# Optimization experiments

Measured on AMD Instinct MI355X. Metric: run time of the kernel, lower is better.

The kernel has to match this reference:

```python
import jax, jax.numpy as jnp
import numpy as np

GROUPS = 32
HEADS = 8
EPS = 1e-5


def group_norm(x, w, b):
    B, C, H, W = x.shape
    xg = x.reshape(B, GROUPS, C // GROUPS, H, W)
    mu = xg.mean(axis=(2, 3, 4), keepdims=True)
    var = xg.var(axis=(2, 3, 4), keepdims=True)
    xn = ((xg - mu) * jax.lax.rsqrt(var + EPS)).reshape(B, C, H, W)
    return xn * w[None, :, None, None] + b[None, :, None, None]


def conv1x1(x, w, b):
    # w: [out_c, in_c], x: [B, C, H, W]
    return jnp.einsum('oc,bchw->bohw', w, x) + b[None, :, None, None]


def setup_inputs() -> dict:
    key = jax.random.key(0)
    ks = jax.random.split(key, 10)
    B, C, H, W = 8, 512, 32, 32
    s = 1.0 / np.sqrt(C)
    inp = {
        'x': jax.random.normal(ks[0], (B, C, H, W), dtype=jnp.float32),
        'gn_w': jnp.ones((C,), jnp.float32),
        'gn_b': jnp.zeros((C,), jnp.float32),
        'qw': jax.random.uniform(ks[1], (C, C), jnp.float32, -s, s),
        'qb': jax.random.uniform(ks[2], (C,), jnp.float32, -s, s),
        'kw': jax.random.uniform(ks[3], (C, C), jnp.float32, -s, s),
        'kb': jax.random.uniform(ks[4], (C,), jnp.float32, -s, s),
        'vw': jax.random.uniform(ks[5], (C, C), jnp.float32, -s, s),
        'vb': jax.random.uniform(ks[6], (C,), jnp.float32, -s, s),
        'ow': jax.random.uniform(ks[7], (C, C), jnp.float32, -s, s),
        'ob': jax.random.uniform(ks[8], (C,), jnp.float32, -s, s),
    }
    return inp


def reference(x, gn_w, gn_b, qw, qb, kw, kb, vw, vb, ow, ob):
    B, C, H, W = x.shape
    hd = C // HEADS          # head_dim
    N = H * W                # spatial tokens
    scale = float(hd) ** -0.5

    xn = group_norm(x, gn_w, gn_b)
    q = conv1x1(xn, qw, qb).reshape(B, HEADS, hd, N)
    k = conv1x1(xn, kw, kb).reshape(B, HEADS, hd, N)
    v = conv1x1(xn, vw, vb).reshape(B, HEADS, hd, N)

    # scores[b,h,n,m] = scale * <q[:, :, :, n], k[:, :, :, m]>
    scores = jnp.einsum('bhdn,bhdm->bhnm', q * scale, k)
    attn = jax.nn.softmax(scores, axis=-1)
    # out[b,h,d,n] = sum_m attn[b,h,n,m] * v[b,h,d,m]
    out = jnp.einsum('bhnm,bhdm->bhdn', attn, v).reshape(B, C, H, W)
    out = conv1x1(out, ow, ob)
    return out + x
```

## Files before the change

kernel.cpp:

```cpp
#include <hip/hip_runtime.h>
#include <cstdint>


typedef unsigned short u16;
typedef __attribute__((ext_vector_type(8))) __bf16 bf16x8;
typedef __attribute__((ext_vector_type(4))) __bf16 bf16x4;
typedef __attribute__((ext_vector_type(4))) float  f32x4;

typedef __attribute__((address_space(1))) const unsigned int guint;
typedef __attribute__((address_space(3))) unsigned int       luint;

__device__ __forceinline__ u16 f2bf(float f) {
  union { float f; unsigned u; } a; a.f = f;
  unsigned r = a.u + 0x7fffu + ((a.u >> 16) & 1u);
  return (u16)(r >> 16);
}

__device__ __forceinline__ void gload16(u16* lds_dst, const u16* g_src) {
  __builtin_amdgcn_global_load_lds((guint*)g_src, (luint*)lds_dst, 16, 0, 0);
}

__global__ __launch_bounds__(256) void gn_stats(const float* __restrict__ x,
                                                float* __restrict__ pstat) {
  int id = blockIdx.x;
  int bg = id >> 1, chunk = id & 1;
  int b = bg >> 5, g = bg & 31;
  int tid = threadIdx.x;
  const float* xg = x + ((size_t)(b * 512 + g * 16 + chunk * 8)) * 1024;
  float s1 = 0.f, s2 = 0.f;
#pragma unroll
  for (int it = 0; it < 8; ++it) {
    f32x4 v = *(const f32x4*)(xg + it * 1024 + tid * 4);
    s1 += (v[0] + v[1]) + (v[2] + v[3]);
    s2 += (v[0] * v[0] + v[1] * v[1]) + (v[2] * v[2] + v[3] * v[3]);
  }
#pragma unroll
  for (int d = 32; d; d >>= 1) { s1 += __shfl_down(s1, d, 64); s2 += __shfl_down(s2, d, 64); }
  __shared__ float redw[4][2];
  if ((tid & 63) == 0) { redw[tid >> 6][0] = s1; redw[tid >> 6][1] = s2; }
  __syncthreads();
  if (tid == 0) {
    float t1 = redw[0][0] + redw[1][0] + redw[2][0] + redw[3][0];
    float t2 = redw[0][1] + redw[1][1] + redw[2][1] + redw[3][1];
    pstat[(bg * 2 + chunk) * 2 + 0] = t1;
    pstat[(bg * 2 + chunk) * 2 + 1] = t2;
  }
}

__global__ __launch_bounds__(256) void gn_apply(const float* __restrict__ x,
                                                const float* __restrict__ pstat,
                                                const float* __restrict__ gw,
                                                const float* __restrict__ gb,
                                                u16* __restrict__ xnT) {
  __shared__ u16 tr[64 * 130];
  int id = blockIdx.x;
  int cs = id & 3, ntl = (id >> 2) & 15, b = id >> 6;
  int tid = threadIdx.x;
  int tc = tid >> 1, th = tid & 1;
  int c = cs * 128 + tc, g = c >> 4;
  float a1 = pstat[(b * 32 + g) * 4 + 0], a2 = pstat[(b * 32 + g) * 4 + 1];
  float b1 = pstat[(b * 32 + g) * 4 + 2], b2 = pstat[(b * 32 + g) * 4 + 3];
  float s1 = a1 + b1, s2 = a2 + b2;
  float mean = s1 * (1.f / 16384.f);
  float var  = s2 * (1.f / 16384.f) - mean * mean;
  float rinv = rsqrtf(var + 1e-5f);
  float wgt = gw[c] * rinv;
  float bia = gb[c] - mean * wgt;
  const float* src = x + ((size_t)(b * 512 + c)) * 1024 + ntl * 64 + th * 32;
#pragma unroll
  for (int i = 0; i < 8; ++i) {
    f32x4 v = *(const f32x4*)(src + i * 4);
#pragma unroll
    for (int j = 0; j < 4; ++j)
      tr[(th * 32 + i * 4 + j) * 130 + tc] = f2bf(v[j] * wgt + bia);
  }
  __syncthreads();
  int n = tid >> 2, q = tid & 3;
  u16* dst = xnT + (size_t)b * 524288 + (size_t)(ntl * 64 + n) * 512 + cs * 128 + q * 32;
#pragma unroll
  for (int wd = 0; wd < 16; ++wd)
    *(unsigned*)&dst[wd * 2] = *(const unsigned*)&tr[n * 130 + q * 32 + wd * 2];
}

__global__ __launch_bounds__(256) void cvtw_kernel(const float* __restrict__ q,
                                                   const float* __restrict__ k,
                                                   const float* __restrict__ v,
                                                   const float* __restrict__ o,
                                                   u16* __restrict__ dst) {
  int i = blockIdx.x * 256 + threadIdx.x;
  int wsel = i >> 16;
  const float* src = wsel == 0 ? q : wsel == 1 ? k : wsel == 2 ? v : o;
  f32x4 val = *(const f32x4*)(src + (size_t)(i & 65535) * 4);
  u16 r0 = f2bf(val[0]), r1 = f2bf(val[1]), r2 = f2bf(val[2]), r3 = f2bf(val[3]);
  unsigned lo = (unsigned)r0 | ((unsigned)r1 << 16);
  unsigned hi = (unsigned)r2 | ((unsigned)r3 << 16);
  unsigned long long pk = (unsigned long long)lo | ((unsigned long long)hi << 32);
  *(unsigned long long*)(dst + (size_t)i * 4) = pk;
}

__global__ __launch_bounds__(256) void gemm_qkv(
    const u16* __restrict__ xnT, const u16* __restrict__ Wc,
    const float* __restrict__ qb, const float* __restrict__ kb,
    const float* __restrict__ vb,
    u16* __restrict__ Qs, u16* __restrict__ Ks, u16* __restrict__ Vs) {
  __shared__ u16 smem[32768];
  int id = blockIdx.x;
  int xcd = id & 7, slot = id >> 3;
  int g12 = slot / 12, q12 = slot % 12;
  int p = xcd * 8 + g12;
  int b = p & 7, yt = p >> 3;
  int xt = q12 & 3, which = q12 >> 2;

  const u16* Ab = xnT + (size_t)b * 524288 + (size_t)yt * 128 * 512;
  const u16* Bb = Wc + which * 262144 + (size_t)xt * 128 * 512;
  const float* bias = which == 0 ? qb : (which == 1 ? kb : vb);
  float scale = which == 0 ? 0.18033688011112043f : 1.0f;

  int tid = threadIdx.x, w = tid >> 6, lane = tid & 63;
  int wr = w >> 1, wcn = w & 1;
  int srow = lane >> 3, sk8 = (lane & 7) ^ srow;
  f32x4 acc[4][4] = {};

#define QKV_STAGE(buf, k0)                                                     \
  {                                                                            \
    u16* lA_ = smem + (buf) * 8192;                                            \
    u16* lB_ = smem + 16384 + (buf) * 8192;                                    \
    _Pragma("unroll")                                                          \
    for (int c2 = 0; c2 < 4; ++c2) {                                           \
      int ck = w * 4 + c2;                                                     \
      gload16(&lA_[ck * 512], Ab + (size_t)(ck * 8 + srow) * 512 + (k0) + sk8 * 8); \
      gload16(&lB_[ck * 512], Bb + (size_t)(ck * 8 + srow) * 512 + (k0) + sk8 * 8); \
    }                                                                          \
  }

  QKV_STAGE(0, 0);
  __syncthreads();
  for (int t = 0; t < 8; ++t) {
    if (t < 7) QKV_STAGE((t + 1) & 1, (t + 1) * 64);
    const u16* lA = smem + (t & 1) * 8192;
    const u16* lB = smem + 16384 + (t & 1) * 8192;
#pragma unroll
    for (int ks = 0; ks < 2; ++ks) {
      int k8 = ks * 4 + (lane >> 4);
      bf16x8 af[4], bfr[4];
#pragma unroll
      for (int mf = 0; mf < 4; ++mf) {
        int row = wr * 64 + mf * 16 + (lane & 15);
        af[mf] = *(const bf16x8*)&lA[row * 64 + ((k8 ^ (row & 7)) * 8)];
      }
#pragma unroll
      for (int nf = 0; nf < 4; ++nf) {
        int row = wcn * 64 + nf * 16 + (lane & 15);
        bfr[nf] = *(const bf16x8*)&lB[row * 64 + ((k8 ^ (row & 7)) * 8)];
      }
#pragma unroll
      for (int mf = 0; mf < 4; ++mf)
#pragma unroll
        for (int nf = 0; nf < 4; ++nf)
          acc[mf][nf] = __builtin_amdgcn_mfma_f32_16x16x32_bf16(af[mf], bfr[nf], acc[mf][nf], 0, 0, 0);
    }
    __syncthreads();
  }
#undef QKV_STAGE

  if (which < 2) {
    u16* dst = (which == 0 ? Qs : Ks) + (size_t)b * 524288;
#pragma unroll
    for (int mf = 0; mf < 4; ++mf)
#pragma unroll
      for (int nf = 0; nf < 4; ++nf) {
        int cc = xt * 128 + wcn * 64 + nf * 16 + (lane & 15);
        float bv = bias[cc];
#pragma unroll
        for (int j = 0; j < 4; ++j) {
          int rr = yt * 128 + wr * 64 + mf * 16 + (lane >> 4) * 4 + j;
          dst[(size_t)rr * 512 + cc] = f2bf((acc[mf][nf][j] + bv) * scale);
        }
      }
  } else {
    u16* tr = smem;
#pragma unroll
    for (int mf = 0; mf < 4; ++mf)
#pragma unroll
      for (int nf = 0; nf < 4; ++nf) {
        int cc_t = wcn * 64 + nf * 16 + (lane & 15);
        float bv = bias[xt * 128 + cc_t];
#pragma unroll
        for (int j = 0; j < 4; ++j) {
          int rr_t = wr * 64 + mf * 16 + (lane >> 4) * 4 + j;
          tr[cc_t * 136 + rr_t] = f2bf(acc[mf][nf][j] + bv);
        }
      }
    __syncthreads();
    int r = tid >> 1, half = tid & 1;
    size_t base = (size_t)b * 524288 + (size_t)(xt * 128 + r) * 1024 + yt * 128 + half * 64;
#pragma unroll
    for (int i = 0; i < 8; ++i) {
      bf16x8 v = *(const bf16x8*)&tr[r * 136 + half * 64 + i * 8];
      *(bf16x8*)&Vs[base + i * 8] = v;
    }
  }
}

__global__ __launch_bounds__(256) void attn_kernel(const u16* __restrict__ Q,
                                                   const u16* __restrict__ Kt,
                                                   const u16* __restrict__ V,
                                                   u16* __restrict__ AO) {
  __shared__ __align__(16) u16 lK[2][4096];
  __shared__ __align__(16) u16 lV[2][4096];
  __shared__ __align__(16) u16 plds[4][2048];
  int id = blockIdx.x;
  int xcd = id & 7, slot = id >> 3;
  int bh = xcd * 8 + (slot >> 3);
  int nt = slot & 7;
  int b = bh >> 3, h = bh & 7;
  int tid = threadIdx.x, w = tid >> 6, lane = tid & 63;
  int ln = lane & 15, hi = lane >> 4;
  int nb = nt * 128 + w * 32;
  const u16* Qb = Q  + (size_t)b * 524288;
  const u16* Kb = Kt + (size_t)b * 524288 + h * 64;
  const u16* Vb = V  + (size_t)b * 524288 + (size_t)(h * 64) * 1024;
  char* pw = (char*)&plds[w][0];
  int srow = lane >> 3, sk8 = (lane & 7) ^ srow;

  int kidx[2][4];
#pragma unroll
  for (int ks = 0; ks < 2; ++ks)
#pragma unroll
    for (int xf = 0; xf < 4; ++xf) {
      int row = xf * 16 + ln;
      kidx[ks][xf] = row * 64 + (((ks * 4 + hi) ^ (row & 7)) * 8);
    }
  int woff[4], roff[2];
#pragma unroll
  for (int nf = 0; nf < 4; ++nf)
    woff[nf] = ln * 128 + ((nf * 32 + hi * 8) ^ ((ln & 7) << 4));
#pragma unroll
  for (int ks = 0; ks < 2; ++ks)
    roff[ks] = ln * 128 + ((ks * 64 + hi * 16) ^ ((ln & 7) << 4));

  bf16x8 bq[2][2];
#pragma unroll
  for (int nq = 0; nq < 2; ++nq)
#pragma unroll
    for (int ks = 0; ks < 2; ++ks)
      bq[nq][ks] = *(const bf16x8*)&Qb[(size_t)(nb + nq * 16 + ln) * 512 +
                                       h * 64 + ks * 32 + hi * 8];

  f32x4 o[2][4] = {};
  float lp[2] = {0.f, 0.f};

#define ATTN_STAGE(buf, m0)                                                    \
  {                                                                            \
    _Pragma("unroll")                                                          \
    for (int c2 = 0; c2 < 2; ++c2) {                                           \
      int ck = w * 2 + c2;                                                     \
      gload16(&lK[buf][ck * 512], Kb + (size_t)((m0) + ck * 8 + srow) * 512 + sk8 * 8); \
      gload16(&lV[buf][ck * 512], Vb + (size_t)(ck * 8 + srow) * 1024 + (m0) + sk8 * 8); \
    }                                                                          \
  }

  ATTN_STAGE(0, 0);
  __syncthreads();
  for (int mt = 0; mt < 16; ++mt) {
    int cur = mt & 1;
    if (mt < 15) ATTN_STAGE(cur ^ 1, (mt + 1) * 64);
    f32x4 s[2][4] = {};
#pragma unroll
    for (int ks = 0; ks < 2; ++ks) {
#pragma unroll
      for (int nf = 0; nf < 4; ++nf) {
        bf16x8 ak = *(const bf16x8*)&lK[cur][kidx[ks][nf]];
        s[0][nf] = __builtin_amdgcn_mfma_f32_16x16x32_bf16(ak, bq[0][ks], s[0][nf], 0, 0, 0);
        s[1][nf] = __builtin_amdgcn_mfma_f32_16x16x32_bf16(ak, bq[1][ks], s[1][nf], 0, 0, 0);
      }
    }
#pragma unroll
    for (int nq = 0; nq < 2; ++nq)
#pragma unroll
      for (int nf = 0; nf < 4; ++nf) {
        float p0 = exp2f(s[nq][nf][0]), p1 = exp2f(s[nq][nf][1]);
        float p2 = exp2f(s[nq][nf][2]), p3 = exp2f(s[nq][nf][3]);
        lp[nq] += (p0 + p1) + (p2 + p3);
        bf16x4 pb;
        pb[0] = (__bf16)p0; pb[1] = (__bf16)p1; pb[2] = (__bf16)p2; pb[3] = (__bf16)p3;
        *(bf16x4*)(pw + nq * 2048 + woff[nf]) = pb;
      }
#pragma unroll
    for (int ks = 0; ks < 2; ++ks) {
      bf16x8 ap0 = *(const bf16x8*)(pw + roff[ks]);
      bf16x8 ap1 = *(const bf16x8*)(pw + 2048 + roff[ks]);
#pragma unroll
      for (int df = 0; df < 4; ++df) {
        bf16x8 bv = *(const bf16x8*)&lV[cur][kidx[ks][df]];
        o[0][df] = __builtin_amdgcn_mfma_f32_16x16x32_bf16(ap0, bv, o[0][df], 0, 0, 0);
        o[1][df] = __builtin_amdgcn_mfma_f32_16x16x32_bf16(ap1, bv, o[1][df], 0, 0, 0);
      }
    }
    __syncthreads();
  }
#undef ATTN_STAGE

#pragma unroll
  for (int nq = 0; nq < 2; ++nq) {
    lp[nq] += __shfl_xor(lp[nq], 16, 64);
    lp[nq] += __shfl_xor(lp[nq], 32, 64);
  }
  float* lf = (float*)pw;
  if (hi == 0) { lf[ln] = lp[0]; lf[16 + ln] = lp[1]; }
  f32x4 lv0 = *(const f32x4*)&lf[hi * 4];
  f32x4 lv1 = *(const f32x4*)&lf[16 + hi * 4];
  float rl[2][4];
#pragma unroll
  for (int j = 0; j < 4; ++j) { rl[0][j] = 1.0f / lv0[j]; rl[1][j] = 1.0f / lv1[j]; }

#pragma unroll
  for (int nq = 0; nq < 2; ++nq)
#pragma unroll
    for (int df = 0; df < 4; ++df)
#pragma unroll
      for (int j = 0; j < 4; ++j) {
        int n = nb + nq * 16 + hi * 4 + j;
        int c = h * 64 + df * 16 + ln;
        AO[(size_t)b * 524288 + (size_t)n * 512 + c] = f2bf(o[nq][df][j] * rl[nq][j]);
      }
}

__global__ __launch_bounds__(256) void gemm_proj(
    const u16* __restrict__ Wo, const u16* __restrict__ AO,
    const float* __restrict__ ob, const float* __restrict__ x,
    float* __restrict__ out) {
  __shared__ u16 smem[24576];
  int id = blockIdx.x;
  int xcd = id & 7, slot = id >> 3;
  int g8 = slot >> 3, y = slot & 7;
  int p = xcd * 8 + g8;
  int b = p & 7, xt = p >> 3;

  const u16* Ab = Wo + (size_t)y * 64 * 512;
  const u16* Bb = AO + (size_t)b * 524288 + (size_t)xt * 128 * 512;

  int tid = threadIdx.x, w = tid >> 6, lane = tid & 63;
  int wr = w >> 1, wcn = w & 1;
  int srow = lane >> 3, sk8 = (lane & 7) ^ srow;
  f32x4 acc[2][4] = {};

#define PROJ_STAGE(buf, k0)                                                    \
  {                                                                            \
    u16* lA_ = smem + (buf) * 4096;                                            \
    u16* lB_ = smem + 8192 + (buf) * 8192;                                     \
    _Pragma("unroll")                                                          \
    for (int c2 = 0; c2 < 6; ++c2) {                                           \
      int ck = w * 6 + c2;                                                     \
      if (ck < 8)                                                              \
        gload16(&lA_[ck * 512], Ab + (size_t)(ck * 8 + srow) * 512 + (k0) + sk8 * 8); \
      else                                                                     \
        gload16(&lB_[(ck - 8) * 512], Bb + (size_t)((ck - 8) * 8 + srow) * 512 + (k0) + sk8 * 8); \
    }                                                                          \
  }

  PROJ_STAGE(0, 0);
  __syncthreads();
  for (int t = 0; t < 8; ++t) {
    if (t < 7) PROJ_STAGE((t + 1) & 1, (t + 1) * 64);
    const u16* lA = smem + (t & 1) * 4096;
    const u16* lB = smem + 8192 + (t & 1) * 8192;
#pragma unroll
    for (int ks = 0; ks < 2; ++ks) {
      int k8 = ks * 4 + (lane >> 4);
      bf16x8 af[2], bfr[4];
#pragma unroll
      for (int mf = 0; mf < 2; ++mf) {
        int row = wr * 32 + mf * 16 + (lane & 15);
        af[mf] = *(const bf16x8*)&lA[row * 64 + ((k8 ^ (row & 7)) * 8)];
      }
#pragma unroll
      for (int nf = 0; nf < 4; ++nf) {
        int row = wcn * 64 + nf * 16 + (lane & 15);
        bfr[nf] = *(const bf16x8*)&lB[row * 64 + ((k8 ^ (row & 7)) * 8)];
      }
#pragma unroll
      for (int mf = 0; mf < 2; ++mf)
#pragma unroll
        for (int nf = 0; nf < 4; ++nf)
          acc[mf][nf] = __builtin_amdgcn_mfma_f32_16x16x32_bf16(af[mf], bfr[nf], acc[mf][nf], 0, 0, 0);
    }
    __syncthreads();
  }
#undef PROJ_STAGE

#pragma unroll
  for (int mf = 0; mf < 2; ++mf)
#pragma unroll
    for (int nf = 0; nf < 4; ++nf) {
      int cc = xt * 128 + wcn * 64 + nf * 16 + (lane & 15);
#pragma unroll
      for (int j = 0; j < 4; ++j) {
        int rr = y * 64 + wr * 32 + mf * 16 + (lane >> 4) * 4 + j;
        size_t idx = (size_t)b * 524288 + (size_t)rr * 1024 + cc;
        out[idx] = acc[mf][nf][j] + ob[rr] + x[idx];
      }
    }
}

extern "C" void kernel_launch(void* const* d_in, const int* in_sizes, int n_in,
                              void* d_out, int out_size, void* d_ws, size_t ws_size,
                              hipStream_t stream) {
  const float* x   = (const float*)d_in[0];
  const float* gnw = (const float*)d_in[1];
  const float* gnb = (const float*)d_in[2];
  const float* qw  = (const float*)d_in[3];
  const float* qb  = (const float*)d_in[4];
  const float* kw  = (const float*)d_in[5];
  const float* kb  = (const float*)d_in[6];
  const float* vw  = (const float*)d_in[7];
  const float* vb  = (const float*)d_in[8];
  const float* ow  = (const float*)d_in[9];
  const float* ob  = (const float*)d_in[10];
  float* out = (float*)d_out;

  u16* ws  = (u16*)d_ws;
  u16* xnT = ws;
  u16* Qs  = ws + 4194304;
  u16* Ks  = ws + 8388608;
  u16* Vs  = ws + 12582912;
  u16* Wc  = ws + 16777216;
  float* pstat = (float*)(ws + 17825792);
  u16* AO  = xnT;

  gn_stats<<<512, 256, 0, stream>>>(x, pstat);
  gn_apply<<<512, 256, 0, stream>>>(x, pstat, gnw, gnb, xnT);
  cvtw_kernel<<<1024, 256, 0, stream>>>(qw, kw, vw, ow, Wc);
  gemm_qkv<<<768, 256, 0, stream>>>(xnT, Wc, qb, kb, vb, Qs, Ks, Vs);
  attn_kernel<<<512, 256, 0, stream>>>(Qs, Ks, Vs, AO);
  gemm_proj<<<512, 256, 0, stream>>>(Wc + 786432, AO, ob, x, out);
}
```

Baseline: 165.8 us.

## Rewrite attention with 32x32 MFMA, in-register P via permlane swap, MFMA rowsum

The attention kernel moves from 16x16x32 to 32x32x16 bf16 MFMA tiles and doubles the K/V tile to 128 keys per stage. The probability tile is packed and rearranged in registers with v_permlane32_swap instead of going through LDS, and the softmax denominator comes from an extra MFMA against a ones vector rather than shuffle reductions. The aim is to cut LDS round trips and sync overhead, at the cost of one extra MFMA per step, more LDS for K/V buffers (lower occupancy) and higher register pressure.

```diff
diff --git a/kernel.cpp b/kernel.cpp
--- a/kernel.cpp
+++ b/kernel.cpp
@@ -3,9 +3,9 @@
 
 
 typedef unsigned short u16;
-typedef __attribute__((ext_vector_type(8))) __bf16 bf16x8;
-typedef __attribute__((ext_vector_type(4))) __bf16 bf16x4;
-typedef __attribute__((ext_vector_type(4))) float  f32x4;
+typedef __attribute__((ext_vector_type(8)))  __bf16 bf16x8;
+typedef __attribute__((ext_vector_type(4)))  float  f32x4;
+typedef __attribute__((ext_vector_type(16))) float  f32x16;
 
 typedef __attribute__((address_space(1))) const unsigned int guint;
 typedef __attribute__((address_space(3))) unsigned int       luint;
@@ -16,6 +16,16 @@
   return (u16)(r >> 16);
 }
 
+__device__ __forceinline__ unsigned pkbf(float a, float b) {
+  unsigned short lo = __builtin_bit_cast(unsigned short, (__bf16)a);
+  unsigned short hi = __builtin_bit_cast(unsigned short, (__bf16)b);
+  return (unsigned)lo | ((unsigned)hi << 16);
+}
+
+__device__ __forceinline__ void plswap(unsigned &a, unsigned &b) {
+  asm("v_permlane32_swap_b32 %0, %1" : "+v"(a), "+v"(b));
+}
+
 __device__ __forceinline__ void gload16(u16* lds_dst, const u16* g_src) {
   __builtin_amdgcn_global_load_lds((guint*)g_src, (luint*)lds_dst, 16, 0, 0);
 }
@@ -24,9 +34,8 @@
                                                 float* __restrict__ pstat) {
   int id = blockIdx.x;
   int bg = id >> 1, chunk = id & 1;
-  int b = bg >> 5, g = bg & 31;
   int tid = threadIdx.x;
-  const float* xg = x + ((size_t)(b * 512 + g * 16 + chunk * 8)) * 1024;
+  const float* xg = x + ((size_t)(bg * 16 + chunk * 8)) * 1024;
   float s1 = 0.f, s2 = 0.f;
 #pragma unroll
   for (int it = 0; it < 8; ++it) {
@@ -206,124 +215,102 @@
                                                    const u16* __restrict__ Kt,
                                                    const u16* __restrict__ V,
                                                    u16* __restrict__ AO) {
-  __shared__ __align__(16) u16 lK[2][4096];
-  __shared__ __align__(16) u16 lV[2][4096];
-  __shared__ __align__(16) u16 plds[4][2048];
+  __shared__ __align__(16) u16 lK[2][8192];
+  __shared__ __align__(16) u16 lV[2][8192];
   int id = blockIdx.x;
   int xcd = id & 7, slot = id >> 3;
   int bh = xcd * 8 + (slot >> 3);
   int nt = slot & 7;
   int b = bh >> 3, h = bh & 7;
   int tid = threadIdx.x, w = tid >> 6, lane = tid & 63;
-  int ln = lane & 15, hi = lane >> 4;
+  int l31 = lane & 31, lh = lane >> 5, r7 = l31 & 7;
   int nb = nt * 128 + w * 32;
   const u16* Qb = Q  + (size_t)b * 524288;
   const u16* Kb = Kt + (size_t)b * 524288 + h * 64;
   const u16* Vb = V  + (size_t)b * 524288 + (size_t)(h * 64) * 1024;
-  char* pw = (char*)&plds[w][0];
-  int srow = lane >> 3, sk8 = (lane & 7) ^ srow;
-
-  int kidx[2][4];
-#pragma unroll
-  for (int ks = 0; ks < 2; ++ks)
-#pragma unroll
-    for (int xf = 0; xf < 4; ++xf) {
-      int row = xf * 16 + ln;
-      kidx[ks][xf] = row * 64 + (((ks * 4 + hi) ^ (row & 7)) * 8);
-    }
-  int woff[4], roff[2];
-#pragma unroll
-  for (int nf = 0; nf < 4; ++nf)
-    woff[nf] = ln * 128 + ((nf * 32 + hi * 8) ^ ((ln & 7) << 4));
-#pragma unroll
-  for (int ks = 0; ks < 2; ++ks)
-    roff[ks] = ln * 128 + ((ks * 64 + hi * 16) ^ ((ln & 7) << 4));
-
-  bf16x8 bq[2][2];
-#pragma unroll
-  for (int nq = 0; nq < 2; ++nq)
-#pragma unroll
-    for (int ks = 0; ks < 2; ++ks)
-      bq[nq][ks] = *(const bf16x8*)&Qb[(size_t)(nb + nq * 16 + ln) * 512 +
-                                       h * 64 + ks * 32 + hi * 8];
-
-  f32x4 o[2][4] = {};
-  float lp[2] = {0.f, 0.f};
+
+  int srowK = lane >> 3, sblkK = (lane & 7) ^ srowK;
+  int srowV = lane >> 4;
+
+  int kblk[4];
+#pragma unroll
+  for (int kc = 0; kc < 4; ++kc) kblk[kc] = ((kc * 2 + lh) ^ r7) * 8;
+
+  bf16x8 bq[4];
+#pragma unroll
+  for (int kc = 0; kc < 4; ++kc)
+    bq[kc] = *(const bf16x8*)&Qb[(size_t)(nb + l31) * 512 + h * 64 + kc * 16 + lh * 8];
+
+  union { unsigned u[4]; bf16x8 v; } uo;
+  uo.u[0] = uo.u[1] = uo.u[2] = uo.u[3] = 0x3F803F80u;
+  bf16x8 vones = uo.v;
+
+  f32x16 o0 = {}, o1 = {}, osum = {};
 
 #define ATTN_STAGE(buf, m0)                                                    \
   {                                                                            \
     _Pragma("unroll")                                                          \
-    for (int c2 = 0; c2 < 2; ++c2) {                                           \
-      int ck = w * 2 + c2;                                                     \
-      gload16(&lK[buf][ck * 512], Kb + (size_t)((m0) + ck * 8 + srow) * 512 + sk8 * 8); \
-      gload16(&lV[buf][ck * 512], Vb + (size_t)(ck * 8 + srow) * 1024 + (m0) + sk8 * 8); \
+    for (int c2 = 0; c2 < 4; ++c2) {                                           \
+      int ck = w * 4 + c2;                                                     \
+      gload16(&lK[buf][ck * 512],                                              \
+              Kb + (size_t)((m0) + ck * 8 + srowK) * 512 + sblkK * 8);         \
+      int rv = ck * 4 + srowV;                                                 \
+      int bvb = (lane & 15) ^ (rv & 7);                                        \
+      gload16(&lV[buf][ck * 512], Vb + (size_t)rv * 1024 + (m0) + bvb * 8);    \
     }                                                                          \
   }
 
   ATTN_STAGE(0, 0);
   __syncthreads();
-  for (int mt = 0; mt < 16; ++mt) {
+  for (int mt = 0; mt < 8; ++mt) {
     int cur = mt & 1;
-    if (mt < 15) ATTN_STAGE(cur ^ 1, (mt + 1) * 64);
-    f32x4 s[2][4] = {};
-#pragma unroll
-    for (int ks = 0; ks < 2; ++ks) {
-#pragma unroll
-      for (int nf = 0; nf < 4; ++nf) {
-        bf16x8 ak = *(const bf16x8*)&lK[cur][kidx[ks][nf]];
-        s[0][nf] = __builtin_amdgcn_mfma_f32_16x16x32_bf16(ak, bq[0][ks], s[0][nf], 0, 0, 0);
-        s[1][nf] = __builtin_amdgcn_mfma_f32_16x16x32_bf16(ak, bq[1][ks], s[1][nf], 0, 0, 0);
-      }
-    }
-#pragma unroll
-    for (int nq = 0; nq < 2; ++nq)
-#pragma unroll
-      for (int nf = 0; nf < 4; ++nf) {
-        float p0 = exp2f(s[nq][nf][0]), p1 = exp2f(s[nq][nf][1]);
-        float p2 = exp2f(s[nq][nf][2]), p3 = exp2f(s[nq][nf][3]);
-        lp[nq] += (p0 + p1) + (p2 + p3);
-        bf16x4 pb;
-        pb[0] = (__bf16)p0; pb[1] = (__bf16)p1; pb[2] = (__bf16)p2; pb[3] = (__bf16)p3;
-        *(bf16x4*)(pw + nq * 2048 + woff[nf]) = pb;
-      }
-#pragma unroll
-    for (int ks = 0; ks < 2; ++ks) {
-      bf16x8 ap0 = *(const bf16x8*)(pw + roff[ks]);
-      bf16x8 ap1 = *(const bf16x8*)(pw + 2048 + roff[ks]);
-#pragma unroll
-      for (int df = 0; df < 4; ++df) {
-        bf16x8 bv = *(const bf16x8*)&lV[cur][kidx[ks][df]];
-        o[0][df] = __builtin_amdgcn_mfma_f32_16x16x32_bf16(ap0, bv, o[0][df], 0, 0, 0);
-        o[1][df] = __builtin_amdgcn_mfma_f32_16x16x32_bf16(ap1, bv, o[1][df], 0, 0, 0);
+    if (mt < 7) ATTN_STAGE(cur ^ 1, (mt + 1) * 128);
+    const u16* kb = lK[cur];
+    const u16* vb = lV[cur];
+#pragma unroll
+    for (int mb = 0; mb < 4; ++mb) {
+      f32x16 s = {};
+      int krow = (mb * 32 + l31) * 64;
+#pragma unroll
+      for (int kc = 0; kc < 4; ++kc) {
+        bf16x8 ak = *(const bf16x8*)&kb[krow + kblk[kc]];
+        s = __builtin_amdgcn_mfma_f32_32x32x16_bf16(ak, bq[kc], s, 0, 0, 0);
+      }
+      float p[16];
+#pragma unroll
+      for (int i = 0; i < 16; ++i) p[i] = exp2f(s[i]);
+      unsigned A0 = pkbf(p[0], p[1]),  B0 = pkbf(p[4], p[5]);
+      unsigned A1 = pkbf(p[2], p[3]),  B1 = pkbf(p[6], p[7]);
+      unsigned A2 = pkbf(p[8], p[9]),  B2 = pkbf(p[12], p[13]);
+      unsigned A3 = pkbf(p[10], p[11]), B3 = pkbf(p[14], p[15]);
+      plswap(A0, B0); plswap(A1, B1); plswap(A2, B2); plswap(A3, B3);
+      union { unsigned u[4]; bf16x8 v; } f0, f1;
+      f0.u[0] = A0; f0.u[1] = A1; f0.u[2] = B0; f0.u[3] = B1;
+      f1.u[0] = A2; f1.u[1] = A3; f1.u[2] = B2; f1.u[3] = B3;
+#pragma unroll
+      for (int kc = 0; kc < 2; ++kc) {
+        bf16x8 pa = kc ? f1.v : f0.v;
+        int vb0 = ((mb * 4 + kc * 2 + lh) ^ r7) * 8;
+        bf16x8 v0 = *(const bf16x8*)&vb[(l31) * 128 + vb0];
+        bf16x8 v1 = *(const bf16x8*)&vb[(32 + l31) * 128 + vb0];
+        o0 = __builtin_amdgcn_mfma_f32_32x32x16_bf16(pa, v0, o0, 0, 0, 0);
+        o1 = __builtin_amdgcn_mfma_f32_32x32x16_bf16(pa, v1, o1, 0, 0, 0);
+        osum = __builtin_amdgcn_mfma_f32_32x32x16_bf16(pa, vones, osum, 0, 0, 0);
       }
     }
     __syncthreads();
   }
 #undef ATTN_STAGE
 
-#pragma unroll
-  for (int nq = 0; nq < 2; ++nq) {
-    lp[nq] += __shfl_xor(lp[nq], 16, 64);
-    lp[nq] += __shfl_xor(lp[nq], 32, 64);
-  }
-  float* lf = (float*)pw;
-  if (hi == 0) { lf[ln] = lp[0]; lf[16 + ln] = lp[1]; }
-  f32x4 lv0 = *(const f32x4*)&lf[hi * 4];
-  f32x4 lv1 = *(const f32x4*)&lf[16 + hi * 4];
-  float rl[2][4];
-#pragma unroll
-  for (int j = 0; j < 4; ++j) { rl[0][j] = 1.0f / lv0[j]; rl[1][j] = 1.0f / lv1[j]; }
-
-#pragma unroll
-  for (int nq = 0; nq < 2; ++nq)
-#pragma unroll
-    for (int df = 0; df < 4; ++df)
-#pragma unroll
-      for (int j = 0; j < 4; ++j) {
-        int n = nb + nq * 16 + hi * 4 + j;
-        int c = h * 64 + df * 16 + ln;
-        AO[(size_t)b * 524288 + (size_t)n * 512 + c] = f2bf(o[nq][df][j] * rl[nq][j]);
-      }
+  size_t base = (size_t)b * 524288;
+#pragma unroll
+  for (int i = 0; i < 16; ++i) {
+    float rl = 1.0f / osum[i];
+    int n = nb + (i & 3) + 8 * (i >> 2) + 4 * lh;
+    size_t rowb = base + (size_t)n * 512 + h * 64;
+    AO[rowb + l31]      = f2bf(o0[i] * rl);
+    AO[rowb + 32 + l31] = f2bf(o1[i] * rl);
+  }
 }
 
 __global__ __launch_bounds__(256) void gemm_proj(
```

New measurement: 166.7 us. About the same (+0.6%).
